# Kernel optimization log

Measured on AMD Instinct MI355X. Metric: run time of the kernel, lower is better.

Reference implementation:

```python
import jax, jax.numpy as jnp
import numpy as np

# block index -> upsample target resolution / whether self-attention is applied
RES = [32, 64, 256, 128, 64, 32, 16, 16, 32, 64, 128, 256]
ATTN = [False, False, False, False, False, True, True, True, True, False, False, False]
EPS = 1e-5


def conv5(x, w, b):
    # valid 5x5 conv, NCHW
    y = jax.lax.conv_general_dilated(x, w, (1, 1), 'VALID',
                                     dimension_numbers=('NCHW', 'OIHW', 'NCHW'))
    return y + b[None, :, None, None]


def up_nearest(x, size):
    # torch nn.Upsample(size) nearest: src_idx = floor(dst_idx * in / out)
    H, W = x.shape[2], x.shape[3]
    ri = (jnp.arange(size) * H) // size
    ci = (jnp.arange(size) * W) // size
    return x[:, :, ri][:, :, :, ci]


def norm_hw(x):
    # InstanceNorm2d(affine=False) == LayerNorm((H,W)) with identity affine:
    # normalize over spatial dims per (N, C), biased variance.
    m = x.mean((2, 3), keepdims=True)
    v = x.var((2, 3), keepdims=True)
    return (x - m) * jax.lax.rsqrt(v + EPS)


def norm_batch(x):
    # BatchNorm2d in training mode: batch statistics over (N, H, W) per channel.
    m = x.mean((0, 2, 3), keepdims=True)
    v = x.var((0, 2, 3), keepdims=True)
    return (x - m) * jax.lax.rsqrt(v + EPS)


def attention(x, qw, qb, kw, kb, vw, vb):
    B, C, H, W = x.shape
    q = (jnp.einsum('oc,bchw->bohw', qw, x) + qb[None, :, None, None]).reshape(B, C, H * W)
    k = (jnp.einsum('oc,bchw->bohw', kw, x) + kb[None, :, None, None]).reshape(B, C, H * W)
    v = (jnp.einsum('oc,bchw->bohw', vw, x) + vb[None, :, None, None]).reshape(B, C, H * W)
    # scores[b, m, n] = sum_c k[b, c, m] * q[b, c, n]; softmax over n
    a = jax.nn.softmax(jnp.einsum('bcm,bcn->bmn', k, q), axis=-1)  # [B, HW, HW]
    out = jnp.einsum('bcm,bmn->bcn', v, a).reshape(B, C, H, W)
    return out + x


def setup_inputs() -> dict:
    key = jax.random.key(0)
    k = jax.random.split(key, 22)
    s = 0.1
    f = jnp.float32
    return {
        'x': jax.random.normal(k[0], (32, 3, 256, 256), f),
        'noise_z': jax.random.normal(k[1], (1, 512), f),
        'lin_w': jax.random.normal(k[2], (768, 512), f) * 0.02,
        'lin_b': jax.random.normal(k[3], (768,), f) * 0.02,
        'conv_w': jax.random.normal(k[4], (12, 3, 3, 5, 5), f) * s,
        'conv_b': jax.random.normal(k[5], (12, 3), f) * s,
        'conv2_w': jax.random.normal(k[6], (12, 3, 3, 5, 5), f) * s,
        'conv2_b': jax.random.normal(k[7], (12, 3), f) * s,
        'q_w': jax.random.normal(k[8], (12, 3, 3), f) * s,
        'q_b': jax.random.normal(k[9], (12, 3), f) * s,
        'k_w': jax.random.normal(k[10], (12, 3, 3), f) * s,
        'k_b': jax.random.normal(k[11], (12, 3), f) * s,
        'v_w': jax.random.normal(k[12], (12, 3, 3), f) * s,
        'v_b': jax.random.normal(k[13], (12, 3), f) * s,
        'in_p': jax.random.uniform(k[14], (12, 3), f),
        'ln_p': jax.random.uniform(k[15], (12, 3), f),
        'bn_p': jax.random.uniform(k[16], (12, 3), f),
        'bn_w': jax.random.uniform(k[17], (12, 3), f),
        'bn_b': jax.random.uniform(k[18], (12, 3), f) * 0.1,
        'p1': jax.random.uniform(k[19], (12,), f),
        'p2': jax.random.uniform(k[20], (12,), f),
    }


def reference(x, noise_z, lin_w, lin_b, conv_w, conv_b, conv2_w, conv2_b,
              q_w, q_b, k_w, k_b, v_w, v_b, in_p, ln_p, bn_p, bn_w, bn_b, p1, p2):

    def block(i, h):
        r = RES[i]
        real = h
        y = up_nearest(conv5(real, conv_w[i], conv_b[i]), r)
        # InstanceNorm / LayerNorm (no affine) coincide here; BatchNorm has affine.
        inorm = norm_hw(y)
        bnorm = norm_batch(y) * bn_w[i][None, :, None, None] + bn_b[i][None, :, None, None]
        y2 = y + (jnp.sum(in_p[i]) + jnp.sum(ln_p[i])) * inorm + jnp.sum(bn_p[i]) * bnorm
        y2 = y2 * p1[i] + p2[i] * up_nearest(conv5(real, conv2_w[i], conv2_b[i]), r)
        if ATTN[i]:
            y2 = attention(y2, q_w[i], q_b[i], k_w[i], k_b[i], v_w[i], v_b[i])
        return y2

    # noise path: Linear(512 -> 768) -> (1, 3, 16, 16) -> ReesBlock(32) -> ReesBlock(64)
    n = (noise_z @ lin_w.T + lin_b).reshape(1, 3, 16, 16)
    n = block(0, n)
    n = block(1, n)  # (1, 3, 64, 64)

    a = x
    for i in range(2, 12):
        a = block(i, a)
        if i == 4:  # encoder index 2, resolution 64 -> add noise (broadcast over batch)
            a = a + n
    return jnp.tanh(a)
```

## Files before the change

### kernel.cpp

```cpp
#include <hip/hip_runtime.h>
#include <math.h>

#define EPS 1e-5f
#define LOG2E 1.44269504088896340736f

#define AS_GLOBAL __attribute__((address_space(1)))
#define AS_LDS    __attribute__((address_space(3)))

__device__ __forceinline__ float2 ab_from(float s1, float s2, float bs, float bs2,
    float hw, float Nf, float si_, float sb, float bnw_c, float bnb_c, float p1v) {
  float inv = 1.0f / hw;
  float mi = s1 * inv, vi = s2 * inv - mi * mi;
  float ri = rsqrtf(vi + EPS);
  float invb = 1.0f / (Nf * hw);
  float mb = bs * invb, vb = bs2 * invb - mb * mb;
  float rb = rsqrtf(vb + EPS);
  float A = 1.0f + si_ * ri + sb * rb * bnw_c;
  float B = -(si_ * ri * mi + sb * rb * bnw_c * mb) + sb * bnb_c;
  return make_float2(A * p1v, B * p1v);
}

__device__ __forceinline__ void compute_AB_P(
    const float* __restrict__ P, int n, int NT, int T, float hw, float Nf,
    const float* __restrict__ inp, const float* __restrict__ lnp,
// ... 119 lines not shown
    int cc = rowlin / IHv, rr = rowlin - cc * IHv;
    int gx2 = sx0 + col2; gx2 = gx2 < Hin ? gx2 : Hin - 1;
    int gy = sy0 + rr; gy = gy < Hin ? gy : Hin - 1;
    lin[(cc * IHv + rr) * IW + col2] =
        stage_val<MODE, IDENT>(inb, ps, pyu, pbase, Hin, gy, gx2, Sp, logrp,
                               pA, pB, pP2v, pnoise, cc);
  }
}

template <int SMODE, int THv>
__global__ __launch_bounds__(256) void conv_up_t(
    const float* __restrict__ in, const float2* __restrict__ pyu,
    float2* __restrict__ yu,
    const float* __restrict__ w1, const float* __restrict__ b1,
    const float* __restrict__ w2, const float* __restrict__ b2,
    float* __restrict__ sums, int Hin, int S, int r, int tilesX, int tilesY,
    const float* __restrict__ psums,
    const float* __restrict__ pinp, const float* __restrict__ plnp,
    const float* __restrict__ pbnp, const float* __restrict__ pbnw,
    const float* __restrict__ pbnb, const float* __restrict__ pp1,
    const float* __restrict__ pp2, const float* __restrict__ pnoise,
    int pN, int Sp, int logrp, int pNT, int pT) {
  const int TW = 64, IW = 68, IH = THv + 4, NH = THv / 16;
  __shared__ float lin[3 * IH * IW];
  __shared__ float pA[3], pB[3], pP2v, sred[12];
  int bid = xcd_swz();
  int tpi = tilesX * tilesY;
  int n = bid / tpi;
  int trem = bid - n * tpi;
  int tyB = trem / tilesX, txB = trem - tyB * tilesX;
  int px0 = txB * TW, py0 = tyB * THv;
  const float* inb = in + (size_t)n * 3 * Hin * Hin;
  if (SMODE == 1) {
    compute_AB_P(psums, n, pNT, pT, (float)(Hin * Hin), (float)pN, pinp, plnp,
                 pbnp, pbnw, pbnb, pp1, pp2, pA, pB, &pP2v, sred);
    size_t pbase = (size_t)n * 3 * Sp * Sp;
    stage_tile<1, false, IH>(lin, nullptr, 0, pyu, pbase, Hin, py0, px0, Sp,
                             logrp, pA, pB, pP2v, pnoise);
  } else if (SMODE == 3) {
    const float* smallb = in + (size_t)n * 3 * Sp * Sp;
    stage_tile<3, false, IH>(lin, smallb, 0, nullptr, 0, Hin, py0, px0, Sp,
                             logrp, nullptr, nullptr, 0.f, nullptr);
  } else {
    if (px0 + IW <= Hin && py0 + IH <= Hin) {
      for (int t4 = threadIdx.x; t4 < 3 * IH * 17; t4 += 256) {
        int cc = t4 / (IH * 17);
        int rem = t4 - cc * (IH * 17);
        int rr = rem / 17, j = rem - rr * 17;
        const float* src = inb + ((size_t)cc * Hin + py0 + rr) * Hin + px0 + 4 * j;
        int base = t4 - (threadIdx.x & 63);
        __builtin_amdgcn_global_load_lds(
            (const AS_GLOBAL void*)src,
            (AS_LDS void*)(lin + 4 * base), 16, 0, 0);
      }
    } else {
      stage_tile<0, false, IH>(lin, inb, 0, nullptr, 0, Hin, py0, px0, 0, 0,
                               nullptr, nullptr, 0.f, nullptr);
    }
  }
  __syncthreads();
  int tx = threadIdx.x & 15, ty = threadIdx.x >> 4;
  int lx0 = tx * 4;
  float a1[NH][3][4], a2[NH][3][4];
  #pragma unroll
  for (int h = 0; h < NH; ++h) {
    #pragma unroll
    for (int c = 0; c < 3; ++c) {
      float bb1 = b1[c], bb2 = b2[c];
      #pragma unroll
      for (int x = 0; x < 4; ++x) { a1[h][c][x] = bb1; a2[h][c][x] = bb2; }
    }
  }
  #pragma unroll 1
  for (int ci = 0; ci < 3; ++ci) {
    const float* wp1 = w1 + ci * 25;
    const float* wp2 = w2 + ci * 25;
    #pragma unroll
    for (int h = 0; h < NH; ++h) {
      const float* lrow = lin + (ci * IH + ty + 16 * h) * IW + lx0;
      float v[5][8];
      #pragma unroll
      for (int ky = 0; ky < 5; ++ky) {
        #pragma unroll
        for (int j = 0; j < 8; ++j) v[ky][j] = lrow[ky * IW + j];
      }
      #pragma unroll
      for (int ky = 0; ky < 5; ++ky) {
        #pragma unroll
        for (int c = 0; c < 3; ++c) {
          #pragma unroll
          for (int kx = 0; kx < 5; ++kx) {
            float wa = wp1[c * 75 + ky * 5 + kx];
            float wb = wp2[c * 75 + ky * 5 + kx];
            #pragma unroll
            for (int x = 0; x < 4; ++x) {
              a1[h][c][x] = fmaf(v[ky][kx + x], wa, a1[h][c][x]);
              a2[h][c][x] = fmaf(v[ky][kx + x], wb, a2[h][c][x]);
            }
          }
        }
      }
    }
  }
  float sc[3] = {0.f, 0.f, 0.f}, sq[3] = {0.f, 0.f, 0.f};
  int hc = S;
  int px = px0 + lx0;
  #pragma unroll
  for (int h = 0; h < NH; ++h) {
    int py = py0 + ty + 16 * h;
    bool valid = (py < S) && (px < S);
    if (valid) {
      float wy = (float)(((py + 1) * r + hc - 1) / hc - (py * r + hc - 1) / hc);
      float wx[4];
      #pragma unroll
      for (int x = 0; x < 4; ++x) {
        int pxx = px + x;
        wx[x] = (float)(((pxx + 1) * r + hc - 1) / hc - (pxx * r + hc - 1) / hc);
      }
      #pragma unroll
      for (int c = 0; c < 3; ++c) {
        size_t idx = ((size_t)(n * 3 + c) * S + py) * S + px;
        float2* yp = yu + idx;
        *reinterpret_cast<float4*>(yp) =
            make_float4(a1[h][c][0], a2[h][c][0], a1[h][c][1], a2[h][c][1]);
        *reinterpret_cast<float4*>(yp + 2) =
            make_float4(a1[h][c][2], a2[h][c][2], a1[h][c][3], a2[h][c][3]);
        #pragma unroll
        for (int x = 0; x < 4; ++x) {
          float wgt = wy * wx[x];
          sc[c] += a1[h][c][x] * wgt;
          sq[c] += a1[h][c][x] * a1[h][c][x] * wgt;
        }
      }
    }
  }
  STATS_REDUCE_STORE(sc, sq, sums, bid)
}

template <int SMODE, bool IDENT>
__global__ __launch_bounds__(256) void conv_dn_t(
    const float* __restrict__ in, const float2* __restrict__ pyu,
    float2* __restrict__ yu,
    const float* __restrict__ w1, const float* __restrict__ b1,
    const float* __restrict__ w2, const float* __restrict__ b2,
    float* __restrict__ sums, int Hin, int S, int hc, int logr,
    int tilesX, int tilesY,
    const float* __restrict__ psums,
    const float* __restrict__ pinp, const float* __restrict__ plnp,
    const float* __restrict__ pbnp, const float* __restrict__ pbnw,
    const float* __restrict__ pbnb, const float* __restrict__ pp1,
    const float* __restrict__ pp2, const float* __restrict__ pnoise,
    int pN, int Sp, int logrp, int pNT, int pT) {
  const int TW = 32, TH = 8, IW = 68, IH = 20;
  __shared__ float lin[3 * IH * IW];
  __shared__ float pA[3], pB[3], pP2v, sred[12];
  int bid = xcd_swz();
  int tpi = tilesX * tilesY;
  int n = bid / tpi;
  int trem = bid - n * tpi;
  int tyB = trem / tilesX, txB = trem - tyB * tilesX;
  int px0 = txB * TW, py0 = tyB * TH;
  int sy0 = (py0 * hc) >> logr, sx0 = (px0 * hc) >> logr;
  const float* inb = in + (size_t)n * 3 * Hin * Hin;
  if (SMODE == 1) {
    compute_AB_P(psums, n, pNT, pT, (float)(Hin * Hin), (float)pN, pinp, plnp,
                 pbnp, pbnw, pbnb, pp1, pp2, pA, pB, &pP2v, sred);
    size_t pbase = (size_t)n * 3 * Sp * Sp;
    stage_tile<1, IDENT, IH>(lin, nullptr, 0, pyu, pbase, Hin, sy0, sx0, Sp,
                             logrp, pA, pB, pP2v, pnoise);
  } else if (SMODE == 2) {
    size_t ps = (size_t)96 * Hin * Hin;
    stage_tile<2, false, IH>(lin, inb, ps, nullptr, 0, Hin, sy0, sx0, 0, 0,
                             nullptr, nullptr, 0.f, nullptr);
  } else {
    stage_tile<0, false, IH>(lin, inb, 0, nullptr, 0, Hin, sy0, sx0, 0, 0,
                             nullptr, nullptr, 0.f, nullptr);
  }
  __syncthreads();
  int tx = threadIdx.x & 31, ty = threadIdx.x >> 5;
  int px = px0 + tx, py = py0 + ty;
  int sxl = ((px * hc) >> logr) - sx0;
  int syl = ((py * hc) >> logr) - sy0;
  float a1[3], a2[3];
  #pragma unroll
  for (int c = 0; c < 3; ++c) { a1[c] = b1[c]; a2[c] = b2[c]; }
  #pragma unroll
  for (int ci = 0; ci < 3; ++ci) {
    const float* lrow = lin + (ci * IH + syl) * IW + sxl;
    const float* wp1 = w1 + ci * 25;
    const float* wp2 = w2 + ci * 25;
    #pragma unroll
    for (int ky = 0; ky < 5; ++ky) {
      float v[5];
      #pragma unroll
      for (int j = 0; j < 5; ++j) v[j] = lrow[ky * IW + j];
      #pragma unroll
      for (int c = 0; c < 3; ++c) {
        #pragma unroll
        for (int kx = 0; kx < 5; ++kx) {
          a1[c] = fmaf(v[kx], wp1[c * 75 + ky * 5 + kx], a1[c]);
          a2[c] = fmaf(v[kx], wp2[c * 75 + ky * 5 + kx], a2[c]);
        }
      }
    }
  }
  float sc[3] = {0.f, 0.f, 0.f}, sq[3] = {0.f, 0.f, 0.f};
  bool valid = (py < S) && (px < S);
  if (valid) {
    #pragma unroll
    for (int c = 0; c < 3; ++c) {
      size_t idx = ((size_t)(n * 3 + c) * S + py) * S + px;
      yu[idx] = make_float2(a1[c], a2[c]);
      sc[c] += a1[c];
      sq[c] += a1[c] * a1[c];
    }
  }
  STATS_REDUCE_STORE(sc, sq, sums, bid)
}

__global__ __launch_bounds__(256) void linear_wave(
    const float* __restrict__ z, const float* __restrict__ w,
    const float* __restrict__ b, float* __restrict__ out) {
  int row = (blockIdx.x << 2) + (threadIdx.x >> 6);
  int lane = threadIdx.x & 63;
  const float4* wr = reinterpret_cast<const float4*>(w + (size_t)row * 512);
  const float4* zz = reinterpret_cast<const float4*>(z);
  float acc = 0.f;
  #pragma unroll
  for (int i = 0; i < 2; ++i) {
    float4 wv = wr[lane + 64 * i];
    float4 zv = zz[lane + 64 * i];
    acc += wv.x * zv.x + wv.y * zv.y + wv.z * zv.z + wv.w * zv.w;
  }
  #pragma unroll
  for (int off = 32; off; off >>= 1) acc += __shfl_down(acc, off);
  if (lane == 0) out[row] = acc + b[row];
}

__global__ __launch_bounds__(256) void noise_rest(
    const float* __restrict__ L0g,
    const float* __restrict__ cw, const float* __restrict__ cb,
    const float* __restrict__ c2w, const float* __restrict__ c2b,
    const float* __restrict__ inp, const float* __restrict__ lnp,
    const float* __restrict__ bnp, const float* __restrict__ bnw,
    const float* __restrict__ bnb, const float* __restrict__ p1p,
    const float* __restrict__ p2p, float* __restrict__ nb0) {
  __shared__ float L0[768];
  __shared__ float ys0[432], u20[432];
  __shared__ float buf1[3072];
  __shared__ float ys1[2352], u21[2352];
  __shared__ float redS[4][3], redQ[4][3];
  __shared__ float AB[6];
  int tid = threadIdx.x;
  for (int t = tid; t < 768; t += 256) L0[t] = L0g[t];
  __syncthreads();
  {
    float sc[3] = {0, 0, 0}, sq[3] = {0, 0, 0};
    for (int p = tid; p < 144; p += 256) {
      int py = p / 12, px = p - py * 12;
      float a1[3], a2[3];
      #pragma unroll
      for (int c = 0; c < 3; ++c) { a1[c] = cb[c]; a2[c] = c2b[c]; }
      for (int ci = 0; ci < 3; ++ci)
        #pragma unroll
        for (int ky = 0; ky < 5; ++ky) {
          const float* row = &L0[ci * 256 + (py + ky) * 16 + px];
          #pragma unroll
          for (int c = 0; c < 3; ++c)
            #pragma unroll
            for (int kx = 0; kx < 5; ++kx) {
              a1[c] = fmaf(row[kx], cw[c * 75 + ci * 25 + ky * 5 + kx], a1[c]);
              a2[c] = fmaf(row[kx], c2w[c * 75 + ci * 25 + ky * 5 + kx], a2[c]);
            }
        }
      int wy = ((py + 1) * 32 + 11) / 12 - (py * 32 + 11) / 12;
      int wx = ((px + 1) * 32 + 11) / 12 - (px * 32 + 11) / 12;
      float wgt = (float)(wy * wx);
      #pragma unroll
      for (int c = 0; c < 3; ++c) {
        ys0[c * 144 + p] = a1[c];
        u20[c * 144 + p] = a2[c];
        sc[c] += a1[c] * wgt;
        sq[c] += a1[c] * a1[c] * wgt;
      }
    }
    #pragma unroll
    for (int off = 32; off; off >>= 1)
      #pragma unroll
      for (int c = 0; c < 3; ++c) {
        sc[c] += __shfl_down(sc[c], off);
        sq[c] += __shfl_down(sq[c], off);
      }
    int wid = tid >> 6, lane = tid & 63;
    if (lane == 0)
      #pragma unroll
      for (int c = 0; c < 3; ++c) { redS[wid][c] = sc[c]; redQ[wid][c] = sq[c]; }
    __syncthreads();
    if (tid < 3) {
      int c = tid;
      float s1 = redS[0][c] + redS[1][c] + redS[2][c] + redS[3][c];
      float s2 = redQ[0][c] + redQ[1][c] + redQ[2][c] + redQ[3][c];
      float si_ = inp[0] + inp[1] + inp[2] + lnp[0] + lnp[1] + lnp[2];
      float sb = bnp[0] + bnp[1] + bnp[2];
      float2 ab = ab_from(s1, s2, s1, s2, 1024.f, 1.f, si_, sb, bnw[c], bnb[c], p1p[0]);
      AB[c] = ab.x; AB[3 + c] = ab.y;
    }
    __syncthreads();
  }
  {
    float P2a = p2p[0];
    for (int t = tid; t < 3072; t += 256) {
      int c = t >> 10, p = t & 1023;
      int oy = p >> 5, ox = p & 31;
      int si = ((oy * 12) >> 5) * 12 + ((ox * 12) >> 5);
      buf1[t] = AB[c] * ys0[c * 144 + si] + AB[3 + c] + P2a * u20[c * 144 + si];
    }
  }
  __syncthreads();
  {
    const float* w1 = cw + 225;
    const float* w2 = c2w + 225;
    float sc[3] = {0, 0, 0}, sq[3] = {0, 0, 0};
    for (int p = tid; p < 784; p += 256) {
      int py = p / 28, px = p - py * 28;
      float a1[3], a2[3];
      #pragma unroll
      for (int c = 0; c < 3; ++c) { a1[c] = cb[3 + c]; a2[c] = c2b[3 + c]; }
      for (int ci = 0; ci < 3; ++ci)
        #pragma unroll
        for (int ky = 0; ky < 5; ++ky) {
          const float* row = &buf1[ci * 1024 + (py + ky) * 32 + px];
          #pragma unroll
          for (int c = 0; c < 3; ++c)
            #pragma unroll
            for (int kx = 0; kx < 5; ++kx) {
              a1[c] = fmaf(row[kx], w1[c * 75 + ci * 25 + ky * 5 + kx], a1[c]);
              a2[c] = fmaf(row[kx], w2[c * 75 + ci * 25 + ky * 5 + kx], a2[c]);
            }
        }
      int wy = ((py + 1) * 64 + 27) / 28 - (py * 64 + 27) / 28;
      int wx = ((px + 1) * 64 + 27) / 28 - (px * 64 + 27) / 28;
      float wgt = (float)(wy * wx);
      #pragma unroll
      for (int c = 0; c < 3; ++c) {
        ys1[c * 784 + p] = a1[c];
        u21[c * 784 + p] = a2[c];
        sc[c] += a1[c] * wgt;
        sq[c] += a1[c] * a1[c] * wgt;
      }
    }
    #pragma unroll
    for (int off = 32; off; off >>= 1)
      #pragma unroll
      for (int c = 0; c < 3; ++c) {
        sc[c] += __shfl_down(sc[c], off);
        sq[c] += __shfl_down(sq[c], off);
      }
    int wid = tid >> 6, lane = tid & 63;
    __syncthreads();
    if (lane == 0)
      #pragma unroll
      for (int c = 0; c < 3; ++c) { redS[wid][c] = sc[c]; redQ[wid][c] = sq[c]; }
    __syncthreads();
    if (tid < 3) {
      int c = tid;
      float s1 = redS[0][c] + redS[1][c] + redS[2][c] + redS[3][c];
      float s2 = redQ[0][c] + redQ[1][c] + redQ[2][c] + redQ[3][c];
      float si_ = inp[3] + inp[4] + inp[5] + lnp[3] + lnp[4] + lnp[5];
      float sb = bnp[3] + bnp[4] + bnp[5];
      float2 ab = ab_from(s1, s2, s1, s2, 4096.f, 1.f, si_, sb, bnw[3 + c], bnb[3 + c], p1p[1]);
      AB[c] = ab.x; AB[3 + c] = ab.y;
    }
    __syncthreads();
  }
  {
    float P2b = p2p[1];
    for (int t = tid; t < 12288; t += 256) {
      int c = t >> 12, p = t & 4095;
      int oy = p >> 6, ox = p & 63;
      int si = ((oy * 28) >> 6) * 28 + ((ox * 28) >> 6);
      nb0[t] = AB[c] * ys1[c * 784 + si] + AB[3 + c] + P2b * u21[c * 784 + si];
    }
  }
}

__global__ __launch_bounds__(256) void attn_rows_f(
    const float2* __restrict__ yu, const float* __restrict__ sums,
    const float* __restrict__ inp, const float* __restrict__ lnp,
    const float* __restrict__ bnp, const float* __restrict__ bnw,
    const float* __restrict__ bnb, const float* __restrict__ p1p,
    const float* __restrict__ p2p,
    const float* __restrict__ qw, const float* __restrict__ qb,
    const float* __restrict__ kw, const float* __restrict__ kb,
    float* __restrict__ Mp, float* __restrict__ Lp, int S,
    int pNT, int pT) {
  __shared__ float pA[3], pB[3], pP2v, sred[12];
  __shared__ __align__(16) float y2s[768], qs[768];
  int bid = blockIdx.x;
  int np = bid & 3; bid >>= 2;
  int mc = bid & 3;
  int b = bid >> 2;
  compute_AB_P(sums, b, pNT, pT, 1024.f, 32.f, inp, lnp, bnp, bnw, bnb, p1p,
               p2p, pA, pB, &pP2v, sred);
  size_t ybase = (size_t)b * 3 * S * S;
  for (int t = threadIdx.x; t < 768; t += 256) {
    int c = t >> 8, j = t & 255;
    int n = (np << 8) + j;
    int oy = n >> 5, ox = n & 31;
    int si = ((oy * S) >> 5) * S + ((ox * S) >> 5);
    float2 v = yu[ybase + c * S * S + si];
    y2s[t] = pA[c] * v.x + pB[c] + pP2v * v.y;
  }
  __syncthreads();
  for (int t = threadIdx.x; t < 768; t += 256) {
    int o = t >> 8, j = t & 255;
    qs[t] = qb[o] + qw[o * 3] * y2s[j] + qw[o * 3 + 1] * y2s[256 + j] +
            qw[o * 3 + 2] * y2s[512 + j];
  }
  __syncthreads();
  int m = (mc << 8) + threadIdx.x;
  int oy = m >> 5, ox = m & 31;
  int si = ((oy * S) >> 5) * S + ((ox * S) >> 5);
  float ym[3];
  #pragma unroll
  for (int c = 0; c < 3; ++c) {
    float2 v = yu[ybase + c * S * S + si];
    ym[c] = pA[c] * v.x + pB[c] + pP2v * v.y;
  }
  float k0 = (kb[0] + kw[0] * ym[0] + kw[1] * ym[1] + kw[2] * ym[2]) * LOG2E;
  float k1 = (kb[1] + kw[3] * ym[0] + kw[4] * ym[1] + kw[5] * ym[2]) * LOG2E;
  float k2 = (kb[2] + kw[6] * ym[0] + kw[7] * ym[1] + kw[8] * ym[2]) * LOG2E;
  const float4* qa4 = reinterpret_cast<const float4*>(qs);
  const float4* qb4 = reinterpret_cast<const float4*>(qs + 256);
  const float4* qc4 = reinterpret_cast<const float4*>(qs + 512);
  float mr = -1e30f;
  #pragma unroll 4
  for (int j = 0; j < 64; ++j) {
    float4 qa = qa4[j], qbv = qb4[j], qc = qc4[j];
    float s0 = k0 * qa.x + k1 * qbv.x + k2 * qc.x;
    float s1 = k0 * qa.y + k1 * qbv.y + k2 * qc.y;
    float s2 = k0 * qa.z + k1 * qbv.z + k2 * qc.z;
    float s3 = k0 * qa.w + k1 * qbv.w + k2 * qc.w;
    mr = fmaxf(mr, fmaxf(fmaxf(s0, s1), fmaxf(s2, s3)));
  }
  float l = 0.f;
// ... 210 lines not shown
      float4 mm = mm4[j], ll = ll4[j];
      float s, w;
      s = ka.x * q0 + kbv.x * q1 + kc.x * q2;
      w = exp2f(s - mm.x) * ll.x;
      a0 = fmaf(va.x, w, a0); a1 = fmaf(vbv.x, w, a1); a2 = fmaf(vc.x, w, a2);
      s = ka.y * q0 + kbv.y * q1 + kc.y * q2;
      w = exp2f(s - mm.y) * ll.y;
      a0 = fmaf(va.y, w, a0); a1 = fmaf(vbv.y, w, a1); a2 = fmaf(vc.y, w, a2);
      s = ka.z * q0 + kbv.z * q1 + kc.z * q2;
      w = exp2f(s - mm.z) * ll.z;
      a0 = fmaf(va.z, w, a0); a1 = fmaf(vbv.z, w, a1); a2 = fmaf(vc.z, w, a2);
      s = ka.w * q0 + kbv.w * q1 + kc.w * q2;
      w = exp2f(s - mm.w) * ll.w;
      a0 = fmaf(va.w, w, a0); a1 = fmaf(vbv.w, w, a1); a2 = fmaf(vc.w, w, a2);
    }
    Oq[tid] = a0;
    Oq[1024 + tid] = a1;
    Oq[2048 + tid] = a2;
  }
  __syncthreads();
  if (tid < 768) {
    int c = tid >> 8, n = tid & 255;
    int cb_ = c << 10;
    y2s[tid] += Oq[cb_ + n] + Oq[cb_ + 256 + n] + Oq[cb_ + 512 + n] + Oq[cb_ + 768 + n];
  }
  __syncthreads();
  float sc[3] = {0.f, 0.f, 0.f}, sq[3] = {0.f, 0.f, 0.f};
  int p = tid;
  if (p < 144) {
    int py = p / 12, px = p - py * 12;
    float a1[3], a2[3];
    #pragma unroll
    for (int c = 0; c < 3; ++c) { a1[c] = cb1[c]; a2[c] = cb2[c]; }
    #pragma unroll
    for (int ci = 0; ci < 3; ++ci) {
      #pragma unroll
      for (int ky = 0; ky < 5; ++ky) {
        const float* row = &y2s[ci * 256 + (py + ky) * 16 + px];
        #pragma unroll
        for (int c = 0; c < 3; ++c) {
          #pragma unroll
          for (int kx = 0; kx < 5; ++kx) {
            a1[c] = fmaf(row[kx], cw1[c * 75 + ci * 25 + ky * 5 + kx], a1[c]);
            a2[c] = fmaf(row[kx], cw2[c * 75 + ci * 25 + ky * 5 + kx], a2[c]);
          }
        }
      }
    }
    float wy = (float)(((py + 1) * r + 11) / 12 - (py * r + 11) / 12);
    float wx = (float)(((px + 1) * r + 11) / 12 - (px * r + 11) / 12);
    float wgt = wy * wx;
    #pragma unroll
    for (int c = 0; c < 3; ++c) {
      yu_out[(size_t)(b * 3 + c) * 144 + p] = make_float2(a1[c], a2[c]);
      sc[c] += a1[c] * wgt;
      sq[c] += a1[c] * a1[c] * wgt;
    }
  }
  #pragma unroll
  for (int off = 32; off; off >>= 1) {
    #pragma unroll
    for (int c = 0; c < 3; ++c) {
      sc[c] += __shfl_down(sc[c], off);
      sq[c] += __shfl_down(sq[c], off);
    }
  }
  int wid = tid >> 6, lane = tid & 63;
  if (lane == 0) {
    #pragma unroll
    for (int c = 0; c < 3; ++c) { redS[wid][c] = sc[c]; redQ[wid][c] = sq[c]; }
  }
  __syncthreads();
  if (tid < 3) {
    int c = tid;
    float s1 = 0.f, s2 = 0.f;
    #pragma unroll
    for (int w = 0; w < 16; ++w) { s1 += redS[w][c]; s2 += redQ[w][c]; }
    int NTg = (int)gridDim.x;
    sums_out[(2 * c) * NTg + b] = s1;
    sums_out[(2 * c + 1) * NTg + b] = s2;
  }
}

__global__ __launch_bounds__(256) void attn144(
    const float2* __restrict__ yu, const float* __restrict__ sums,
    const float* __restrict__ inp, const float* __restrict__ lnp,
    const float* __restrict__ bnp, const float* __restrict__ bnw,
    const float* __restrict__ bnb, const float* __restrict__ p1p,
    const float* __restrict__ p2p,
    const float* __restrict__ qw, const float* __restrict__ qb,
    const float* __restrict__ kw, const float* __restrict__ kb,
    const float* __restrict__ vw, const float* __restrict__ vb,
    float* __restrict__ O) {
  __shared__ float pA[3], pB[3], pP2v, sred[12];
  __shared__ float y2[432], qs[432], ks[432], vs[432];
  __shared__ float Ms[144], Ls[144], wn[144];
  int b = blockIdx.x;
  int tid = threadIdx.x;
  compute_AB_P(sums, b, 32, 1, 1024.f, 32.f, inp, lnp, bnp, bnw, bnb, p1p,
               p2p, pA, pB, &pP2v, sred);
  for (int t = tid; t < 432; t += 256) {
    int c = t / 144, j = t - c * 144;
    float2 v = yu[((size_t)b * 3 + c) * 144 + j];
    y2[t] = pA[c] * v.x + pB[c] + pP2v * v.y;
  }
  __syncthreads();
  if (tid < 144) {
    int j = tid;
    float y0 = y2[j], y1 = y2[144 + j], y2v = y2[288 + j];
    #pragma unroll
    for (int o = 0; o < 3; ++o) {
      qs[o * 144 + j] = qb[o] + qw[o * 3] * y0 + qw[o * 3 + 1] * y1 + qw[o * 3 + 2] * y2v;
      ks[o * 144 + j] = (kb[o] + kw[o * 3] * y0 + kw[o * 3 + 1] * y1 + kw[o * 3 + 2] * y2v) * LOG2E;
      vs[o * 144 + j] = vb[o] + vw[o * 3] * y0 + vw[o * 3 + 1] * y1 + vw[o * 3 + 2] * y2v;
    }
    int jy = j / 12, jx = j - jy * 12;
    int cy = (8 * (jy + 1) + 2) / 3 - (8 * jy + 2) / 3;
    int cx = (8 * (jx + 1) + 2) / 3 - (8 * jx + 2) / 3;
    wn[j] = (float)(cy * cx);
  }
  __syncthreads();
  if (tid < 144) {
    int m = tid;
    float kx = ks[m], ky = ks[144 + m], kz = ks[288 + m];
    float mr = -1e30f;
    for (int nn = 0; nn < 144; ++nn) {
      float s = kx * qs[nn] + ky * qs[144 + nn] + kz * qs[288 + nn];
      mr = fmaxf(mr, s);
    }
    float l = 0.f;
    for (int nn = 0; nn < 144; ++nn) {
      float s = kx * qs[nn] + ky * qs[144 + nn] + kz * qs[288 + nn];
      l += wn[nn] * exp2f(s - mr);
    }
    Ms[m] = mr;
    Ls[m] = 1.0f / l;
  }
  __syncthreads();
  if (tid < 144) {
    int nq = tid;
    float q0 = qs[nq], q1 = qs[144 + nq], q2 = qs[288 + nq];
    float a0 = 0.f, a1 = 0.f, a2 = 0.f;
    for (int m = 0; m < 144; ++m) {
      float s = ks[m] * q0 + ks[144 + m] * q1 + ks[288 + m] * q2;
      float w = wn[m] * exp2f(s - Ms[m]) * Ls[m];
      a0 = fmaf(vs[m], w, a0);
      a1 = fmaf(vs[144 + m], w, a1);
      a2 = fmaf(vs[288 + m], w, a2);
    }
    size_t ob = (size_t)b * 432;
    O[ob + nq] = a0 + y2[nq];
    O[ob + 144 + nq] = a1 + y2[144 + nq];
    O[ob + 288 + nq] = a2 + y2[288 + nq];
  }
}

__global__ __launch_bounds__(256) void elem_final(
    const float2* __restrict__ yu, const float* __restrict__ sums,
    const float* __restrict__ inp, const float* __restrict__ lnp,
    const float* __restrict__ bnp, const float* __restrict__ bnw,
    const float* __restrict__ bnb, const float* __restrict__ p1p,
    const float* __restrict__ p2p, float* __restrict__ out, int S,
    int pNT, int pT) {
  __shared__ float pA[3], pB[3], pP2v, sred[12];
  int bid = xcd_swz();
  int n = bid >> 6;
  int part = bid & 63;
  compute_AB_P(sums, n, pNT, pT, 65536.f, 32.f, inp, lnp, bnp, bnw, bnb, p1p,
               p2p, pA, pB, &pP2v, sred);
  int p0 = (part << 10) + ((int)threadIdx.x << 2);
  int oy = p0 >> 8;
  int oxb = p0 & 255;
  int sy = ((oy * S) >> 8) * S;
  int si0 = sy + ((oxb * S) >> 8);
  int si1 = sy + (((oxb + 1) * S) >> 8);
  int si2 = sy + (((oxb + 2) * S) >> 8);
  int si3 = sy + (((oxb + 3) * S) >> 8);
  size_t ybase = (size_t)n * 3 * S * S;
  #pragma unroll
  for (int c = 0; c < 3; ++c) {
    const float2* yp = yu + ybase + (size_t)c * S * S;
    float2 v0 = yp[si0], v1 = yp[si1], v2 = yp[si2], v3 = yp[si3];
    float4 r;
    r.x = tanhf(pA[c] * v0.x + pB[c] + pP2v * v0.y);
    r.y = tanhf(pA[c] * v1.x + pB[c] + pP2v * v1.y);
    r.z = tanhf(pA[c] * v2.x + pB[c] + pP2v * v2.y);
    r.w = tanhf(pA[c] * v3.x + pB[c] + pP2v * v3.y);
    *reinterpret_cast<float4*>(&out[((size_t)(n * 3 + c) << 16) + p0]) = r;
  }
}

#define NPX nullptr, nullptr, nullptr, nullptr, nullptr, nullptr, nullptr, \
            nullptr, nullptr, 0, 0, 0, 0, 0

extern "C" void kernel_launch(void* const* d_in, const int* in_sizes, int n_in,
                              void* d_out, int out_size, void* d_ws, size_t ws_size,
                              hipStream_t stream) {
  const float* x       = (const float*)d_in[0];
  const float* noise_z = (const float*)d_in[1];
  const float* lin_w   = (const float*)d_in[2];
  const float* lin_b   = (const float*)d_in[3];
  const float* conv_w  = (const float*)d_in[4];
  const float* conv_b  = (const float*)d_in[5];
  const float* conv2_w = (const float*)d_in[6];
  const float* conv2_b = (const float*)d_in[7];
  const float* q_w     = (const float*)d_in[8];
  const float* q_b     = (const float*)d_in[9];
  const float* k_w     = (const float*)d_in[10];
  const float* k_b     = (const float*)d_in[11];
  const float* v_w     = (const float*)d_in[12];
  const float* v_b     = (const float*)d_in[13];
  const float* in_p    = (const float*)d_in[14];
  const float* ln_p    = (const float*)d_in[15];
  const float* bn_p    = (const float*)d_in[16];
  const float* bn_w    = (const float*)d_in[17];
  const float* bn_b    = (const float*)d_in[18];
  const float* p1      = (const float*)d_in[19];
  const float* p2      = (const float*)d_in[20];
  float* out = (float*)d_out;

  float* ws = (float*)d_ws;
  size_t off = 0;
  auto alloc = [&](size_t nf) { float* p = ws + off; off += nf; return p; };
  float* PS    = alloc(27264);
  float* PS2   = PS;
  float* PS3   = PS + 6144;
  float* PS4   = PS + 18432;
  float* PS5   = PS + 21504;
  float* PS6   = PS + 22272;
  float* PS6a  = PS + 22656;
  float* PS7a  = PS + 22848;
  float* PS9   = PS + 23040;
  float* PS10  = PS + 23424;
  float* PS11  = PS + 24192;
  float* P45  = alloc(393216);
  float* O144 = alloc(13824);
  float2* YU2 = (float2*)alloc(12192768);
  float2* PA  = (float2*)alloc(3145728);
  float2* PB  = (float2*)alloc(3145728);
  float* Mp   = alloc(131072);
  float* Lp   = alloc(131072);
  float* NB0  = alloc(12288);
  float* LIN  = alloc(768);

  const float* nul = nullptr;
  const float2* nul2 = nullptr;

  linear_wave<<<192, 256, 0, stream>>>(noise_z, lin_w, lin_b, LIN);
  noise_rest<<<1, 256, 0, stream>>>(LIN, conv_w, conv_b, conv2_w, conv2_b,
      in_p, ln_p, bn_p, bn_w, bn_b, p1, p2, NB0);

  conv_up_t<0, 32><<<1024, 256, 0, stream>>>(x, nul2, YU2, conv_w + 450,
      conv_b + 6, conv2_w + 450, conv2_b + 6, PS2, 256, 252, 256, 4, 8,
      NPX);
  conv_dn_t<1, false><<<2048, 256, 0, stream>>>(nul, YU2, PA,
      conv_w + 675, conv_b + 9, conv2_w + 675, conv2_b + 9, PS3,
      256, 128, 252, 7, 4, 16,
      PS2, in_p + 6, ln_p + 6, bn_p + 6, bn_w + 6, bn_b + 6, p1 + 2,
      p2 + 2, nul, 32, 252, 8, 1024, 32);
  conv_dn_t<1, true><<<512, 256, 0, stream>>>(nul, PA, PB,
      conv_w + 900, conv_b + 12, conv2_w + 900, conv2_b + 12, PS4,
      128, 64, 124, 6, 2, 8,
      PS3, in_p + 9, ln_p + 9, bn_p + 9, bn_w + 9, bn_b + 9, p1 + 3,
      p2 + 3, nul, 32, 128, 7, 2048, 64);
  conv_dn_t<1, true><<<128, 256, 0, stream>>>(nul, PB, PA,
      conv_w + 1125, conv_b + 15, conv2_w + 1125, conv2_b + 15, PS5,
      64, 32, 60, 5, 1, 4,
      PS4, in_p + 12, ln_p + 12, bn_p + 12, bn_w + 12, bn_b + 12, p1 + 4,
      p2 + 4, NB0, 32, 64, 6, 512, 16);
  attn_rows_f<<<512, 256, 0, stream>>>(PA, PS5, in_p + 15, ln_p + 15,
      bn_p + 15, bn_w + 15, bn_b + 15, p1 + 5, p2 + 5,
      q_w + 45, q_b + 15, k_w + 45, k_b + 15, Mp, Lp, 32, 128, 4);
  attn_out_f<<<512, 256, 0, stream>>>(PA, PS5, in_p + 15, ln_p + 15,
      bn_p + 15, bn_w + 15, bn_b + 15, p1 + 5, p2 + 5,
      q_w + 45, q_b + 15, k_w + 45, k_b + 15, v_w + 45, v_b + 15, Mp, Lp, P45,
      32, 128, 4);
  conv_dn_t<2, false><<<64, 256, 0, stream>>>(P45, nul2, PB,
      conv_w + 1350, conv_b + 18, conv2_w + 1350, conv2_b + 18, PS6,
      32, 16, 28, 4, 1, 2, NPX);
  attn256_conv<<<32, 1024, 0, stream>>>(PB, PS6, in_p + 18, ln_p + 18,
      bn_p + 18, bn_w + 18, bn_b + 18, p1 + 6, p2 + 6,
      q_w + 54, q_b + 18, k_w + 54, k_b + 18, v_w + 54, v_b + 18,
      conv_w + 1575, conv_b + 21, conv2_w + 1575, conv2_b + 21,
      PA, PS6a, 16, 16, 64, 2);
  attn256_conv<<<32, 1024, 0, stream>>>(PA, PS6a, in_p + 21, ln_p + 21,
      bn_p + 21, bn_w + 21, bn_b + 21, p1 + 7, p2 + 7,
      q_w + 63, q_b + 21, k_w + 63, k_b + 21, v_w + 63, v_b + 21,
      conv_w + 1800, conv_b + 24, conv2_w + 1800, conv2_b + 24,
      PB, PS7a, 12, 32, 32, 1);
  attn144<<<32, 256, 0, stream>>>(PB, PS7a, in_p + 24, ln_p + 24,
      bn_p + 24, bn_w + 24, bn_b + 24, p1 + 8, p2 + 8,
      q_w + 72, q_b + 24, k_w + 72, k_b + 24, v_w + 72, v_b + 24, O144);
  conv_up_t<3, 16><<<64, 256, 0, stream>>>(O144, nul2, PA, conv_w + 2025,
      conv_b + 27, conv2_w + 2025, conv2_b + 27, PS9, 32, 28, 64, 1, 2,
      nullptr, nullptr, nullptr, nullptr, nullptr, nullptr, nullptr,
      nullptr, nullptr, 0, 12, 5, 0, 0);
  conv_up_t<1, 16><<<128, 256, 0, stream>>>(nul, PA, PB, conv_w + 2250,
      conv_b + 30, conv2_w + 2250, conv2_b + 30, PS10, 64, 60, 128, 1, 4,
      PS9, in_p + 27, ln_p + 27, bn_p + 27, bn_w + 27, bn_b + 27,
      p1 + 9, p2 + 9, nul, 32, 28, 6, 64, 2);
  conv_up_t<1, 16><<<512, 256, 0, stream>>>(nul, PB, YU2, conv_w + 2475,
      conv_b + 33, conv2_w + 2475, conv2_b + 33, PS11, 128, 124, 256, 2, 8,
      PS10, in_p + 30, ln_p + 30, bn_p + 30, bn_w + 30, bn_b + 30,
      p1 + 10, p2 + 10, nul, 32, 60, 7, 128, 4);
  elem_final<<<2048, 256, 0, stream>>>(YU2, PS11, in_p + 33, ln_p + 33,
      bn_p + 33, bn_w + 33, bn_b + 33, p1 + 11, p2 + 11, out, 124, 512, 16);
}
```

Before: 419.3 us.

## Fuse noise linear into noise kernel and block-9 conv into attn144

The separate linear_wave kernel is folded into the single-block noise kernel, which now computes the 768-row matvec with four waves before the noise convolutions. The block-9 conv/upsample stage (previously conv_up_t on O144) is moved into the attention kernel, so each batch block convolves its attention output directly from shared memory and writes yu plus per-block stats. The changed stats layout is reflected in the downstream kernel's arguments. This removes two launches and an intermediate buffer round trip. The cost is that one block now does all 768 linear rows serially, and the conv runs on only 32 blocks.

```diff
diff --git a/kernel.cpp b/kernel.cpp
--- a/kernel.cpp
+++ b/kernel.cpp
@@ -225,7 +225,7 @@
       #pragma unroll
       for (int ky = 0; ky < 5; ++ky) {
         #pragma unroll
-        for (int j = 0; j < 8; ++j) v[ky][j] = lrow[ky * IW + j];
+        for (int j = 0; j < 8; ++j) { v[ky][j] = lrow[ky * IW + j]; }
       }
       #pragma unroll
       for (int ky = 0; ky < 5; ++ky) {
@@ -336,7 +336,7 @@
     for (int ky = 0; ky < 5; ++ky) {
       float v[5];
       #pragma unroll
-      for (int j = 0; j < 5; ++j) v[j] = lrow[ky * IW + j];
+      for (int j = 0; j < 5; ++j) { v[j] = lrow[ky * IW + j]; }
       #pragma unroll
       for (int c = 0; c < 3; ++c) {
         #pragma unroll
@@ -361,27 +361,9 @@
   STATS_REDUCE_STORE(sc, sq, sums, bid)
 }
 
-__global__ __launch_bounds__(256) void linear_wave(
-    const float* __restrict__ z, const float* __restrict__ w,
-    const float* __restrict__ b, float* __restrict__ out) {
-  int row = (blockIdx.x << 2) + (threadIdx.x >> 6);
-  int lane = threadIdx.x & 63;
-  const float4* wr = reinterpret_cast<const float4*>(w + (size_t)row * 512);
-  const float4* zz = reinterpret_cast<const float4*>(z);
-  float acc = 0.f;
-  #pragma unroll
-  for (int i = 0; i < 2; ++i) {
-    float4 wv = wr[lane + 64 * i];
-    float4 zv = zz[lane + 64 * i];
-    acc += wv.x * zv.x + wv.y * zv.y + wv.z * zv.z + wv.w * zv.w;
-  }
-  #pragma unroll
-  for (int off = 32; off; off >>= 1) acc += __shfl_down(acc, off);
-  if (lane == 0) out[row] = acc + b[row];
-}
-
-__global__ __launch_bounds__(256) void noise_rest(
-    const float* __restrict__ L0g,
+__global__ __launch_bounds__(256) void noise_all(
+    const float* __restrict__ z, const float* __restrict__ lw,
+    const float* __restrict__ lb,
     const float* __restrict__ cw, const float* __restrict__ cb,
     const float* __restrict__ c2w, const float* __restrict__ c2b,
     const float* __restrict__ inp, const float* __restrict__ lnp,
@@ -395,7 +377,21 @@
   __shared__ float redS[4][3], redQ[4][3];
   __shared__ float AB[6];
   int tid = threadIdx.x;
-  for (int t = tid; t < 768; t += 256) L0[t] = L0g[t];
+  {
+    int wid = tid >> 6, lane = tid & 63;
+    const float4* zz = reinterpret_cast<const float4*>(z);
+    float4 zv0 = zz[lane], zv1 = zz[lane + 64];
+    for (int row = wid; row < 768; row += 4) {
+      const float4* wr = reinterpret_cast<const float4*>(lw + (size_t)row * 512);
+      float4 wv0 = wr[lane];
+      float4 wv1 = wr[lane + 64];
+      float acc = wv0.x * zv0.x + wv0.y * zv0.y + wv0.z * zv0.z + wv0.w * zv0.w +
+                  wv1.x * zv1.x + wv1.y * zv1.y + wv1.z * zv1.z + wv1.w * zv1.w;
+      #pragma unroll
+      for (int off = 32; off; off >>= 1) { acc += __shfl_down(acc, off); }
+      if (lane == 0) L0[row] = acc + lb[row];
+    }
+  }
   __syncthreads();
   {
     float sc[3] = {0, 0, 0}, sq[3] = {0, 0, 0};
@@ -404,18 +400,20 @@
       float a1[3], a2[3];
       #pragma unroll
       for (int c = 0; c < 3; ++c) { a1[c] = cb[c]; a2[c] = c2b[c]; }
-      for (int ci = 0; ci < 3; ++ci)
+      for (int ci = 0; ci < 3; ++ci) {
         #pragma unroll
         for (int ky = 0; ky < 5; ++ky) {
           const float* row = &L0[ci * 256 + (py + ky) * 16 + px];
           #pragma unroll
-          for (int c = 0; c < 3; ++c)
+          for (int c = 0; c < 3; ++c) {
             #pragma unroll
             for (int kx = 0; kx < 5; ++kx) {
               a1[c] = fmaf(row[kx], cw[c * 75 + ci * 25 + ky * 5 + kx], a1[c]);
               a2[c] = fmaf(row[kx], c2w[c * 75 + ci * 25 + ky * 5 + kx], a2[c]);
             }
+          }
         }
+      }
       int wy = ((py + 1) * 32 + 11) / 12 - (py * 32 + 11) / 12;
       int wx = ((px + 1) * 32 + 11) / 12 - (px * 32 + 11) / 12;
       float wgt = (float)(wy * wx);
@@ -428,16 +426,18 @@
       }
     }
     #pragma unroll
-    for (int off = 32; off; off >>= 1)
+    for (int off = 32; off; off >>= 1) {
       #pragma unroll
       for (int c = 0; c < 3; ++c) {
         sc[c] += __shfl_down(sc[c], off);
         sq[c] += __shfl_down(sq[c], off);
       }
+    }
     int wid = tid >> 6, lane = tid & 63;
-    if (lane == 0)
+    if (lane == 0) {
       #pragma unroll
       for (int c = 0; c < 3; ++c) { redS[wid][c] = sc[c]; redQ[wid][c] = sq[c]; }
+    }
     __syncthreads();
     if (tid < 3) {
       int c = tid;
@@ -469,18 +469,20 @@
       float a1[3], a2[3];
       #pragma unroll
       for (int c = 0; c < 3; ++c) { a1[c] = cb[3 + c]; a2[c] = c2b[3 + c]; }
-      for (int ci = 0; ci < 3; ++ci)
+      for (int ci = 0; ci < 3; ++ci) {
         #pragma unroll
         for (int ky = 0; ky < 5; ++ky) {
           const float* row = &buf1[ci * 1024 + (py + ky) * 32 + px];
           #pragma unroll
-          for (int c = 0; c < 3; ++c)
+          for (int c = 0; c < 3; ++c) {
             #pragma unroll
             for (int kx = 0; kx < 5; ++kx) {
               a1[c] = fmaf(row[kx], w1[c * 75 + ci * 25 + ky * 5 + kx], a1[c]);
               a2[c] = fmaf(row[kx], w2[c * 75 + ci * 25 + ky * 5 + kx], a2[c]);
             }
+          }
         }
+      }
       int wy = ((py + 1) * 64 + 27) / 28 - (py * 64 + 27) / 28;
       int wx = ((px + 1) * 64 + 27) / 28 - (px * 64 + 27) / 28;
       float wgt = (float)(wy * wx);
@@ -493,17 +495,19 @@
       }
     }
     #pragma unroll
-    for (int off = 32; off; off >>= 1)
+    for (int off = 32; off; off >>= 1) {
       #pragma unroll
       for (int c = 0; c < 3; ++c) {
         sc[c] += __shfl_down(sc[c], off);
         sq[c] += __shfl_down(sq[c], off);
       }
+    }
     int wid = tid >> 6, lane = tid & 63;
     __syncthreads();
-    if (lane == 0)
+    if (lane == 0) {
       #pragma unroll
       for (int c = 0; c < 3; ++c) { redS[wid][c] = sc[c]; redQ[wid][c] = sq[c]; }
+    }
     __syncthreads();
     if (tid < 3) {
       int c = tid;
@@ -880,8 +884,8 @@
   }
 }
 
-__global__ __launch_bounds__(256) void attn144(
-    const float2* __restrict__ yu, const float* __restrict__ sums,
+__global__ __launch_bounds__(256) void attn144c9_k(
+    const float2* __restrict__ yin, const float* __restrict__ sums,
     const float* __restrict__ inp, const float* __restrict__ lnp,
     const float* __restrict__ bnp, const float* __restrict__ bnw,
     const float* __restrict__ bnb, const float* __restrict__ p1p,
@@ -889,22 +893,24 @@
     const float* __restrict__ qw, const float* __restrict__ qb,
     const float* __restrict__ kw, const float* __restrict__ kb,
     const float* __restrict__ vw, const float* __restrict__ vb,
-    float* __restrict__ O) {
+    const float* __restrict__ cw1, const float* __restrict__ cb1,
+    const float* __restrict__ cw2, const float* __restrict__ cb2,
+    float2* __restrict__ yu_out, float* __restrict__ sums_out) {
   __shared__ float pA[3], pB[3], pP2v, sred[12];
   __shared__ float y2[432], qs[432], ks[432], vs[432];
-  __shared__ float Ms[144], Ls[144], wn[144];
+  __shared__ float Msa[144], Lsa[144], wn[144], Osh[432];
   int b = blockIdx.x;
-  int tid = threadIdx.x;
+  int t = threadIdx.x;
   compute_AB_P(sums, b, 32, 1, 1024.f, 32.f, inp, lnp, bnp, bnw, bnb, p1p,
                p2p, pA, pB, &pP2v, sred);
-  for (int t = tid; t < 432; t += 256) {
-    int c = t / 144, j = t - c * 144;
-    float2 v = yu[((size_t)b * 3 + c) * 144 + j];
-    y2[t] = pA[c] * v.x + pB[c] + pP2v * v.y;
-  }
-  __syncthreads();
-  if (tid < 144) {
-    int j = tid;
+  for (int idx = t; idx < 432; idx += 256) {
+    int c = idx / 144, j = idx - c * 144;
+    float2 v = yin[(size_t)(b * 3 + c) * 144 + j];
+    y2[idx] = pA[c] * v.x + pB[c] + pP2v * v.y;
+  }
+  __syncthreads();
+  if (t < 144) {
+    int j = t;
     float y0 = y2[j], y1 = y2[144 + j], y2v = y2[288 + j];
     #pragma unroll
     for (int o = 0; o < 3; ++o) {
@@ -918,8 +924,8 @@
     wn[j] = (float)(cy * cx);
   }
   __syncthreads();
-  if (tid < 144) {
-    int m = tid;
+  if (t < 144) {
+    int m = t;
     float kx = ks[m], ky = ks[144 + m], kz = ks[288 + m];
     float mr = -1e30f;
     for (int nn = 0; nn < 144; ++nn) {
@@ -931,26 +937,62 @@
       float s = kx * qs[nn] + ky * qs[144 + nn] + kz * qs[288 + nn];
       l += wn[nn] * exp2f(s - mr);
     }
-    Ms[m] = mr;
-    Ls[m] = 1.0f / l;
-  }
-  __syncthreads();
-  if (tid < 144) {
-    int nq = tid;
+    Msa[m] = mr;
+    Lsa[m] = 1.0f / l;
+  }
+  __syncthreads();
+  if (t < 144) {
+    int nq = t;
     float q0 = qs[nq], q1 = qs[144 + nq], q2 = qs[288 + nq];
     float a0 = 0.f, a1 = 0.f, a2 = 0.f;
     for (int m = 0; m < 144; ++m) {
       float s = ks[m] * q0 + ks[144 + m] * q1 + ks[288 + m] * q2;
-      float w = wn[m] * exp2f(s - Ms[m]) * Ls[m];
+      float w = wn[m] * exp2f(s - Msa[m]) * Lsa[m];
       a0 = fmaf(vs[m], w, a0);
       a1 = fmaf(vs[144 + m], w, a1);
       a2 = fmaf(vs[288 + m], w, a2);
     }
-    size_t ob = (size_t)b * 432;
-    O[ob + nq] = a0 + y2[nq];
-    O[ob + 144 + nq] = a1 + y2[144 + nq];
-    O[ob + 288 + nq] = a2 + y2[288 + nq];
-  }
+    Osh[nq] = a0 + y2[nq];
+    Osh[144 + nq] = a1 + y2[144 + nq];
+    Osh[288 + nq] = a2 + y2[288 + nq];
+  }
+  __syncthreads();
+  float sc[3] = {0.f, 0.f, 0.f}, sq[3] = {0.f, 0.f, 0.f};
+  for (int o = t; o < 784; o += 256) {
+    int py = o / 28, px = o - py * 28;
+    float a1[3], a2[3];
+    #pragma unroll
+    for (int c = 0; c < 3; ++c) { a1[c] = cb1[c]; a2[c] = cb2[c]; }
+    #pragma unroll
+    for (int ci = 0; ci < 3; ++ci) {
+      const float* obase = &Osh[ci * 144];
+      #pragma unroll
+      for (int ky = 0; ky < 5; ++ky) {
+        int sy = ((py + ky) * 12) >> 5;
+        const float* orow = obase + sy * 12;
+        #pragma unroll
+        for (int kx = 0; kx < 5; ++kx) {
+          int sx = ((px + kx) * 12) >> 5;
+          float v = orow[sx];
+          #pragma unroll
+          for (int c = 0; c < 3; ++c) {
+            a1[c] = fmaf(v, cw1[c * 75 + ci * 25 + ky * 5 + kx], a1[c]);
+            a2[c] = fmaf(v, cw2[c * 75 + ci * 25 + ky * 5 + kx], a2[c]);
+          }
+        }
+      }
+    }
+    float wy = (float)(((py + 1) * 64 + 27) / 28 - (py * 64 + 27) / 28);
+    float wx = (float)(((px + 1) * 64 + 27) / 28 - (px * 64 + 27) / 28);
+    float wgt = wy * wx;
+    #pragma unroll
+    for (int c = 0; c < 3; ++c) {
+      yu_out[((size_t)(b * 3 + c) * 28 + py) * 28 + px] = make_float2(a1[c], a2[c]);
+      sc[c] += a1[c] * wgt;
+      sq[c] += a1[c] * a1[c] * wgt;
+    }
+  }
+  STATS_REDUCE_STORE(sc, sq, sums_out, b)
 }
 
 __global__ __launch_bounds__(256) void elem_final(
@@ -1032,20 +1074,18 @@
   float* PS10  = PS + 23424;
   float* PS11  = PS + 24192;
   float* P45  = alloc(393216);
-  float* O144 = alloc(13824);
   float2* YU2 = (float2*)alloc(12192768);
   float2* PA  = (float2*)alloc(3145728);
   float2* PB  = (float2*)alloc(3145728);
   float* Mp   = alloc(131072);
   float* Lp   = alloc(131072);
   float* NB0  = alloc(12288);
-  float* LIN  = alloc(768);
 
   const float* nul = nullptr;
   const float2* nul2 = nullptr;
 
-  linear_wave<<<192, 256, 0, stream>>>(noise_z, lin_w, lin_b, LIN);
-  noise_rest<<<1, 256, 0, stream>>>(LIN, conv_w, conv_b, conv2_w, conv2_b,
+  noise_all<<<1, 256, 0, stream>>>(noise_z, lin_w, lin_b,
+      conv_w, conv_b, conv2_w, conv2_b,
       in_p, ln_p, bn_p, bn_w, bn_b, p1, p2, NB0);
 
   conv_up_t<0, 32><<<1024, 256, 0, stream>>>(x, nul2, YU2, conv_w + 450,
@@ -1086,17 +1126,15 @@
       q_w + 63, q_b + 21, k_w + 63, k_b + 21, v_w + 63, v_b + 21,
       conv_w + 1800, conv_b + 24, conv2_w + 1800, conv2_b + 24,
       PB, PS7a, 12, 32, 32, 1);
-  attn144<<<32, 256, 0, stream>>>(PB, PS7a, in_p + 24, ln_p + 24,
+  attn144c9_k<<<32, 256, 0, stream>>>(PB, PS7a, in_p + 24, ln_p + 24,
       bn_p + 24, bn_w + 24, bn_b + 24, p1 + 8, p2 + 8,
-      q_w + 72, q_b + 24, k_w + 72, k_b + 24, v_w + 72, v_b + 24, O144);
-  conv_up_t<3, 16><<<64, 256, 0, stream>>>(O144, nul2, PA, conv_w + 2025,
-      conv_b + 27, conv2_w + 2025, conv2_b + 27, PS9, 32, 28, 64, 1, 2,
-      nullptr, nullptr, nullptr, nullptr, nullptr, nullptr, nullptr,
-      nullptr, nullptr, 0, 12, 5, 0, 0);
+      q_w + 72, q_b + 24, k_w + 72, k_b + 24, v_w + 72, v_b + 24,
+      conv_w + 2025, conv_b + 27, conv2_w + 2025, conv2_b + 27,
+      PA, PS9);
   conv_up_t<1, 16><<<128, 256, 0, stream>>>(nul, PA, PB, conv_w + 2250,
       conv_b + 30, conv2_w + 2250, conv2_b + 30, PS10, 64, 60, 128, 1, 4,
       PS9, in_p + 27, ln_p + 27, bn_p + 27, bn_w + 27, bn_b + 27,
-      p1 + 9, p2 + 9, nul, 32, 28, 6, 64, 2);
+      p1 + 9, p2 + 9, nul, 32, 28, 6, 32, 1);
   conv_up_t<1, 16><<<512, 256, 0, stream>>>(nul, PB, YU2, conv_w + 2475,
       conv_b + 33, conv2_w + 2475, conv2_b + 33, PS11, 128, 124, 256, 2, 8,
       PS10, in_p + 30, ln_p + 30, bn_p + 30, bn_w + 30, bn_b + 30,
```

Measured after the change: 533.9 us. 27.4% more time.
